# Optimization experiments

Measured on AMD Instinct MI355X. Metric: run time of the kernel, lower is better.

## Reference

```python
import jax, jax.numpy as jnp
import numpy as np

D_MODEL = 1024
N_HEADS = 16
HEAD_DIM = D_MODEL // N_HEADS


def setup_inputs() -> dict:
    key = jax.random.key(0)
    k0, k1, k2, k3, k4, k5 = jax.random.split(key, 6)
    s = 1.0 / np.sqrt(D_MODEL)
    return {
        "q": jax.random.normal(k0, (2, 2048, D_MODEL), dtype=jnp.float32),
        "Wq": jax.random.normal(k1, (D_MODEL, D_MODEL), dtype=jnp.float32) * s,
        "Wk": jax.random.normal(k2, (D_MODEL, D_MODEL), dtype=jnp.float32) * s,
        "Wv": jax.random.normal(k3, (D_MODEL, D_MODEL), dtype=jnp.float32) * s,
        "Wo": jax.random.normal(k4, (D_MODEL, D_MODEL), dtype=jnp.float32) * s,
        "bo": jax.random.normal(k5, (D_MODEL,), dtype=jnp.float32) * 0.01,
    }


def _split_heads(x):
    b, s, _ = x.shape
    return x.reshape(b, s, N_HEADS, HEAD_DIM).transpose(0, 2, 1, 3)  # [b,h,s,d]


def reference(q, Wq, Wk, Wv, Wo, bo):
    # self-attention: k = v = q
    qh = _split_heads(q @ Wq)  # [b,h,s,d]
    kh = _split_heads(q @ Wk)
    vh = _split_heads(q @ Wv)
    scale = 1.0 / np.sqrt(HEAD_DIM).astype(np.float32)
    scores = jnp.einsum("bhqd,bhkd->bhqk", qh, kh) * scale
    attn = jax.nn.softmax(scores, axis=-1)
    ctx = jnp.einsum("bhqk,bhkd->bhqd", attn, vh)
    b, h, s, d = ctx.shape
    ctx = ctx.transpose(0, 2, 1, 3).reshape(b, s, h * d)
    return ctx @ Wo + bo
```

## Files before the change

### kernel.cpp

```cpp
#include <hip/hip_runtime.h>
#include <cstdint>

typedef unsigned short u16;
typedef __bf16 bf16x8 __attribute__((ext_vector_type(8)));
typedef __bf16 bf16x2 __attribute__((ext_vector_type(2)));
typedef float floatx4 __attribute__((ext_vector_type(4)));
typedef unsigned short u16x4 __attribute__((ext_vector_type(4)));
typedef unsigned short u16x8 __attribute__((ext_vector_type(8)));

#define MFMA16(a, b, c) __builtin_amdgcn_mfma_f32_16x16x32_bf16((a), (b), (c), 0, 0, 0)
#define QSCALE_LOG2E 0.18033688011112042f


typedef __attribute__((address_space(3))) void as3_void;
typedef __attribute__((address_space(1))) void as1_void;

static __device__ __forceinline__ void async_load16(const void* g, void* l) {
  __builtin_amdgcn_global_load_lds((as1_void*)(uintptr_t)g, (as3_void*)(uintptr_t)l,
                                   16, 0, 0);
}

static __device__ __forceinline__ u16 f2bf(float f) {
  union { float f; unsigned int u; } v; v.f = f;
  unsigned int u = v.u;
  u += 0x7fffu + ((u >> 16) & 1u);
  return (u16)(u >> 16);
}

static __device__ __forceinline__ u16x4 pack_bf4(float a, float b, float c, float d) {
#if __has_builtin(__builtin_amdgcn_cvt_pk_bf16_f32)
  union { u16x4 v4; bf16x2 v2[2]; } u;
  u.v2[0] = __builtin_amdgcn_cvt_pk_bf16_f32(a, b);
  u.v2[1] = __builtin_amdgcn_cvt_pk_bf16_f32(c, d);
  return u.v4;
#else
  u16x4 r; r[0] = f2bf(a); r[1] = f2bf(b); r[2] = f2bf(c); r[3] = f2bf(d);
  return r;
#endif
}

static __device__ __forceinline__ float fast_exp2(float x) {
#if __has_builtin(__builtin_amdgcn_exp2f)
  return __builtin_amdgcn_exp2f(x);
#else
  return exp2f(x);
#endif
}


__global__ __launch_bounds__(256) void prep_kernel(
    const float* __restrict__ w0, const float* __restrict__ w1,
    const float* __restrict__ w2, const float* __restrict__ w3,
    u16* __restrict__ wout,
    const float* __restrict__ xin, u16* __restrict__ xout) {
  if (blockIdx.z == 4) {
    int blk = blockIdx.y * 16 + blockIdx.x;
    size_t base = (size_t)blk * 16384 + (size_t)threadIdx.x * 8;
#pragma unroll
    for (int r = 0; r < 8; r++) {
      size_t i = base + (size_t)r * 2048;
      float4 a = *(const float4*)(xin + i);
      float4 b = *(const float4*)(xin + i + 4);
      u16x8 o;
      o[0] = f2bf(a.x); o[1] = f2bf(a.y); o[2] = f2bf(a.z); o[3] = f2bf(a.w);
      o[4] = f2bf(b.x); o[5] = f2bf(b.y); o[6] = f2bf(b.z); o[7] = f2bf(b.w);
      *(u16x8*)(xout + i) = o;
    }
    return;
  }
  __shared__ u16 t[64][65];
  const float* in = (blockIdx.z == 0) ? w0 : (blockIdx.z == 1) ? w1
                    : (blockIdx.z == 2) ? w2 : w3;
  u16* oz = wout + (size_t)blockIdx.z * (1024 * 1024);
  const int tid = threadIdx.x;
  const int x = tid & 63, y0 = tid >> 6;
  const int bx = blockIdx.x * 64, by = blockIdx.y * 64;
#pragma unroll
  for (int p = 0; p < 16; p++) {
    int y = y0 + p * 4;
    t[y][x] = f2bf(in[(size_t)(by + y) * 1024 + bx + x]);
  }
  __syncthreads();
#pragma unroll
  for (int p = 0; p < 16; p++) {
    int r = y0 + p * 4;
    oz[(size_t)(bx + r) * 1024 + by + x] = t[x][r];
  }
}


__global__ __launch_bounds__(256) void vt_kernel(
    const u16* __restrict__ V, u16* __restrict__ VT) {
  __shared__ u16 t[64][65];
  const int bh = blockIdx.z, b = bh >> 4, h = bh & 15;
  const u16* iz = V + (size_t)b * 2048 * 1024 + h * 64;
  u16* oz = VT + (size_t)bh * 64 * 2048;
  const int tid = threadIdx.x;
  const int x = tid & 63, y0 = tid >> 6;
  const int by = blockIdx.y * 64;
#pragma unroll
  for (int p = 0; p < 16; p++) {
    int y = y0 + p * 4;
    t[y][x] = iz[(size_t)(by + y) * 1024 + x];
  }
  __syncthreads();
#pragma unroll
  for (int p = 0; p < 16; p++) {
    int r = y0 + p * 4;
    oz[(size_t)r * 2048 + by + x] = t[x][r];
  }
}


__global__ __launch_bounds__(256, 2) void gemm_bt_kernel(
    const u16* __restrict__ A, const u16* __restrict__ BT,
    const float* __restrict__ bias, void* __restrict__ out,
    int M, int N, int K, int mode) {
  __shared__ u16 As[128 * 32];
  __shared__ u16 Bs[128 * 32];
  const int tid = threadIdx.x;
  const int w = tid >> 6, lane = tid & 63;
  const int bm = blockIdx.y * 128, bn = blockIdx.x * 128;
  const int z = blockIdx.z;
  const u16* Bz = BT + (size_t)z * N * K;

  const int c0 = w * 2, c1 = c0 + 1;
  const int mA0 = c0 * 16 + (lane >> 2), mA1 = c1 * 16 + (lane >> 2);
  const int kg0 = (lane & 3) ^ ((mA0 >> 1) & 3);
  const int kg1 = (lane & 3) ^ ((mA1 >> 1) & 3);
  const u16* agp0 = A + (size_t)(bm + mA0) * K + kg0 * 8;
  const u16* agp1 = A + (size_t)(bm + mA1) * K + kg1 * 8;
  const u16* bgp0 = Bz + (size_t)(bn + mA0) * K + kg0 * 8;
  const u16* bgp1 = Bz + (size_t)(bn + mA1) * K + kg1 * 8;
  u16* ald0 = As + c0 * 512; u16* ald1 = As + c1 * 512;
  u16* bld0 = Bs + c0 * 512; u16* bld1 = Bs + c1 * 512;

  const int wm = (w >> 1) * 64, wn = (w & 1) * 64;
  floatx4 acc[4][4] = {};

  int a_off[4], b_off[4];
#pragma unroll
  for (int i = 0; i < 4; i++) {
    int m = wm + i * 16 + (lane & 15);
    a_off[i] = m * 32 + (((lane >> 4) ^ ((m >> 1) & 3)) * 8);
    int n = wn + i * 16 + (lane & 15);
    b_off[i] = n * 32 + (((lane >> 4) ^ ((n >> 1) & 3)) * 8);
  }

  for (int k0 = 0; k0 < K; k0 += 32) {
    __syncthreads();
    async_load16(agp0 + k0, ald0);
    async_load16(agp1 + k0, ald1);
    async_load16(bgp0 + k0, bld0);
    async_load16(bgp1 + k0, bld1);
    __syncthreads();
    bf16x8 af[4], bf[4];
#pragma unroll
    for (int i = 0; i < 4; i++) af[i] = *(const bf16x8*)(As + a_off[i]);
#pragma unroll
    for (int j = 0; j < 4; j++) bf[j] = *(const bf16x8*)(Bs + b_off[j]);
#pragma unroll
    for (int i = 0; i < 4; i++)
#pragma unroll
      for (int j = 0; j < 4; j++)
        acc[i][j] = MFMA16(af[i], bf[j], acc[i][j]);
  }

  const int roff = (lane >> 4) * 4;
  const int coff = lane & 15;
  if (mode == 0) {
    const float sc = (z == 0) ? QSCALE_LOG2E : 1.0f;
    u16* outz = (u16*)out + (size_t)z * M * N;
#pragma unroll
    for (int i = 0; i < 4; i++) {
      int r0 = bm + wm + i * 16 + roff;
#pragma unroll
      for (int j = 0; j < 4; j++) {
        int c = bn + wn + j * 16 + coff;
#pragma unroll
        for (int r = 0; r < 4; r++)
          outz[(size_t)(r0 + r) * N + c] = f2bf(acc[i][j][r] * sc);
      }
    }
  } else {
    float* outf = (float*)out;
#pragma unroll
    for (int i = 0; i < 4; i++) {
      int r0 = bm + wm + i * 16 + roff;
#pragma unroll
      for (int j = 0; j < 4; j++) {
        int c = bn + wn + j * 16 + coff;
        float bv = bias[c];
#pragma unroll
        for (int r = 0; r < 4; r++)
          outf[(size_t)(r0 + r) * N + c] = acc[i][j][r] + bv;
      }
    }
  }
}


__global__ __launch_bounds__(256, 2) void attn_kernel(
    const u16* __restrict__ Q, const u16* __restrict__ Kx,
    const u16* __restrict__ VT, u16* __restrict__ ctx) {
  __shared__ u16 Ks[128 * 64];
  __shared__ u16 Vs[64 * 128];
  __shared__ u16 Ps[4][32 * 136];
  const int tid = threadIdx.x;
  const int w = tid >> 6, lane = tid & 63;
  const int bh = blockIdx.y, b = bh >> 4, h = bh & 15;
  const int q0 = blockIdx.x * 128;
  const u16* Qh = Q + (size_t)b * 2048 * 1024 + h * 64;
  const u16* Kh = Kx + (size_t)b * 2048 * 1024 + h * 64;
  const u16* Vh = VT + (size_t)bh * 64 * 2048;

  const int qbase = q0 + w * 32;
  bf16x8 qf[2][2];
#pragma unroll
  for (int qt = 0; qt < 2; qt++)
#pragma unroll
    for (int ks = 0; ks < 2; ks++)
      qf[qt][ks] = *(const bf16x8*)(Qh + (size_t)(qbase + qt * 16 + (lane & 15)) * 1024 +
                                    ks * 32 + (lane >> 4) * 8);

  bf16x8 onesf;
#pragma unroll
  for (int i = 0; i < 8; i++) onesf[i] = (__bf16)1.0f;

  const u16* kgp[4]; const u16* vgp[4];
  u16* kld[4]; u16* vld[4];
#pragma unroll
  for (int i = 0; i < 4; i++) {
    int c = w * 4 + i;
    int sl = c * 8 + (lane >> 3);
    int dg = (lane & 7) ^ (lane >> 3);
    kgp[i] = Kh + (size_t)sl * 1024 + dg * 8;
    kld[i] = Ks + c * 512;
    int dl = c * 4 + (lane >> 4);
    int sg = (lane & 15) ^ (dl & 15);
    vgp[i] = Vh + (size_t)dl * 2048 + sg * 8;
    vld[i] = Vs + c * 512;
  }

  floatx4 o[2][4] = {};
  floatx4 lacc[2] = {};
  u16* Pw = Ps[w];

  for (int t = 0; t < 16; t++) {
    const int k0 = t * 128;
    __syncthreads();
#pragma unroll
    for (int i = 0; i < 4; i++) {
      async_load16(kgp[i] + (size_t)k0 * 1024, kld[i]);
      async_load16(vgp[i] + k0, vld[i]);
    }
    __syncthreads();

    floatx4 st[8][2];
#pragma unroll
    for (int si = 0; si < 8; si++) {
      st[si][0] = floatx4{0.f, 0.f, 0.f, 0.f};
      st[si][1] = floatx4{0.f, 0.f, 0.f, 0.f};
    }
#pragma unroll
    for (int ks = 0; ks < 2; ks++) {
#pragma unroll
      for (int si = 0; si < 8; si++) {
        int s = si * 16 + (lane & 15);
        int slot = ((ks * 4) + (lane >> 4)) ^ (s & 7);
        bf16x8 kf = *(const bf16x8*)(Ks + s * 64 + slot * 8);
        st[si][0] = MFMA16(kf, qf[0][ks], st[si][0]);
        st[si][1] = MFMA16(kf, qf[1][ks], st[si][1]);
      }
    }

#pragma unroll
    for (int qt = 0; qt < 2; qt++) {
      int q = qt * 16 + (lane & 15);
#pragma unroll
      for (int si = 0; si < 8; si++) {
        float p0 = fast_exp2(st[si][qt][0]);
        float p1 = fast_exp2(st[si][qt][1]);
        float p2 = fast_exp2(st[si][qt][2]);
        float p3 = fast_exp2(st[si][qt][3]);
        u16x4 pk = pack_bf4(p0, p1, p2, p3);
        *(u16x4*)(Pw + q * 136 + si * 16 + (lane >> 4) * 4) = pk;
      }
    }

#pragma unroll
    for (int ks = 0; ks < 4; ks++) {
      bf16x8 vf[4];
#pragma unroll
      for (int jt = 0; jt < 4; jt++) {
        int d = jt * 16 + (lane & 15);
        int slot = ((ks * 4) + (lane >> 4)) ^ (d & 15);
        vf[jt] = *(const bf16x8*)(Vs + d * 128 + slot * 8);
      }
#pragma unroll
      for (int qt = 0; qt < 2; qt++) {
        bf16x8 pf = *(const bf16x8*)(Pw + (qt * 16 + (lane & 15)) * 136 +
                                     ks * 32 + (lane >> 4) * 8);
#pragma unroll
        for (int jt = 0; jt < 4; jt++)
          o[qt][jt] = MFMA16(pf, vf[jt], o[qt][jt]);
        lacc[qt] = MFMA16(pf, onesf, lacc[qt]);
      }
    }
  }

#pragma unroll
  for (int qt = 0; qt < 2; qt++)
#pragma unroll
    for (int r = 0; r < 4; r++) {
      float inv = 1.0f / lacc[qt][r];
      int s = qbase + qt * 16 + (lane >> 4) * 4 + r;
#pragma unroll
      for (int j = 0; j < 4; j++) {
        int c = h * 64 + j * 16 + (lane & 15);
        ctx[(size_t)(b * 2048 + s) * 1024 + c] = f2bf(o[qt][j][r] * inv);
      }
    }
}


extern "C" void kernel_launch(void* const* d_in, const int* in_sizes, int n_in,
                              void* d_out, int out_size, void* d_ws, size_t ws_size,
                              hipStream_t stream) {
  (void)in_sizes; (void)n_in; (void)out_size; (void)ws_size;
  const float* x  = (const float*)d_in[0];
  const float* Wq = (const float*)d_in[1];
  const float* Wk = (const float*)d_in[2];
  const float* Wv = (const float*)d_in[3];
  const float* Wo = (const float*)d_in[4];
  const float* bo = (const float*)d_in[5];
  u16* ws = (u16*)d_ws;
  const size_t MM = 1024 * 1024;
  u16* WT  = ws;
  u16* WoT = ws + 3 * MM;
  u16* Xb  = ws + 4 * MM;
  u16* QKV = ws + 8 * MM;
  u16* VTp = ws + 20 * MM;
  u16* CTX = ws + 24 * MM;

  dim3 blk(256);
  prep_kernel<<<dim3(16, 16, 5), blk, 0, stream>>>(Wq, Wk, Wv, Wo, WT, x, Xb);
  gemm_bt_kernel<<<dim3(8, 32, 3), blk, 0, stream>>>(Xb, WT, nullptr, QKV,
                                                     4096, 1024, 1024, 0);
  vt_kernel<<<dim3(1, 32, 32), blk, 0, stream>>>(QKV + 8 * MM, VTp);
  attn_kernel<<<dim3(16, 32, 1), blk, 0, stream>>>(QKV, QKV + 4 * MM, VTp, CTX);
  gemm_bt_kernel<<<dim3(8, 32, 1), blk, 0, stream>>>(CTX, WoT, bo, d_out,
                                                     4096, 1024, 1024, 1);
}
```

Before: 197.7 us.

## Fuse V transpose into QKV GEMM epilogue, remap attention grid, restructure score loop

The QKV projection GEMM now writes the V output transposed per head straight into the VT buffer, which removes the separate vt_kernel launch and its round trip through memory. The attention grid is flattened to 1D and remapped so that groups of 8 heads share consecutive block ids, aiming for better K/V cache locality across concurrently running blocks. The QK^T score loop is restructured to compute, exponentiate and store P per 16-key tile with precomputed LDS base pointers, which shortens register live ranges. The GEMM launch bound is raised to 3 blocks per SM, which may force register spills.

```diff
diff --git a/kernel.cpp b/kernel.cpp
--- a/kernel.cpp
+++ b/kernel.cpp
@@ -89,32 +89,10 @@
 }
 
 
-__global__ __launch_bounds__(256) void vt_kernel(
-    const u16* __restrict__ V, u16* __restrict__ VT) {
-  __shared__ u16 t[64][65];
-  const int bh = blockIdx.z, b = bh >> 4, h = bh & 15;
-  const u16* iz = V + (size_t)b * 2048 * 1024 + h * 64;
-  u16* oz = VT + (size_t)bh * 64 * 2048;
-  const int tid = threadIdx.x;
-  const int x = tid & 63, y0 = tid >> 6;
-  const int by = blockIdx.y * 64;
-#pragma unroll
-  for (int p = 0; p < 16; p++) {
-    int y = y0 + p * 4;
-    t[y][x] = iz[(size_t)(by + y) * 1024 + x];
-  }
-  __syncthreads();
-#pragma unroll
-  for (int p = 0; p < 16; p++) {
-    int r = y0 + p * 4;
-    oz[(size_t)r * 2048 + by + x] = t[x][r];
-  }
-}
-
-
-__global__ __launch_bounds__(256, 2) void gemm_bt_kernel(
+__global__ __launch_bounds__(256, 3) void gemm_bt_kernel(
     const u16* __restrict__ A, const u16* __restrict__ BT,
     const float* __restrict__ bias, void* __restrict__ out,
+    u16* __restrict__ outVT,
     int M, int N, int K, int mode) {
   __shared__ u16 As[128 * 32];
   __shared__ u16 Bs[128 * 32];
@@ -169,17 +147,32 @@
   const int roff = (lane >> 4) * 4;
   const int coff = lane & 15;
   if (mode == 0) {
-    const float sc = (z == 0) ? QSCALE_LOG2E : 1.0f;
-    u16* outz = (u16*)out + (size_t)z * M * N;
-#pragma unroll
-    for (int i = 0; i < 4; i++) {
-      int r0 = bm + wm + i * 16 + roff;
-#pragma unroll
-      for (int j = 0; j < 4; j++) {
-        int c = bn + wn + j * 16 + coff;
-#pragma unroll
-        for (int r = 0; r < 4; r++)
-          outz[(size_t)(r0 + r) * N + c] = f2bf(acc[i][j][r] * sc);
+    if (z == 2) {
+#pragma unroll
+      for (int i = 0; i < 4; i++) {
+        int r0 = bm + wm + i * 16 + roff;
+        int b = r0 >> 11, s = r0 & 2047;
+#pragma unroll
+        for (int j = 0; j < 4; j++) {
+          int c = bn + wn + j * 16 + coff;
+          int h = c >> 6, d = c & 63;
+          u16x4 pk = pack_bf4(acc[i][j][0], acc[i][j][1], acc[i][j][2], acc[i][j][3]);
+          *(u16x4*)(outVT + ((size_t)(b * 16 + h) * 64 + d) * 2048 + s) = pk;
+        }
+      }
+    } else {
+      const float sc = (z == 0) ? QSCALE_LOG2E : 1.0f;
+      u16* outz = (u16*)out + (size_t)z * M * N;
+#pragma unroll
+      for (int i = 0; i < 4; i++) {
+        int r0 = bm + wm + i * 16 + roff;
+#pragma unroll
+        for (int j = 0; j < 4; j++) {
+          int c = bn + wn + j * 16 + coff;
+#pragma unroll
+          for (int r = 0; r < 4; r++)
+            outz[(size_t)(r0 + r) * N + c] = f2bf(acc[i][j][r] * sc);
+        }
       }
     }
   } else {
@@ -208,8 +201,10 @@
   __shared__ u16 Ps[4][32 * 136];
   const int tid = threadIdx.x;
   const int w = tid >> 6, lane = tid & 63;
-  const int bh = blockIdx.y, b = bh >> 4, h = bh & 15;
-  const int q0 = blockIdx.x * 128;
+  const int bid = blockIdx.x;
+  const int bh = (bid >> 7) * 8 + (bid & 7);
+  const int q0 = ((bid >> 3) & 15) * 128;
+  const int b = bh >> 4, h = bh & 15;
   const u16* Qh = Q + (size_t)b * 2048 * 1024 + h * 64;
   const u16* Kh = Kx + (size_t)b * 2048 * 1024 + h * 64;
   const u16* Vh = VT + (size_t)bh * 64 * 2048;
@@ -226,6 +221,7 @@
   bf16x8 onesf;
 #pragma unroll
   for (int i = 0; i < 8; i++) onesf[i] = (__bf16)1.0f;
+  const floatx4 zero4 = {};
 
   const u16* kgp[4]; const u16* vgp[4];
   u16* kld[4]; u16* vld[4];
@@ -242,6 +238,11 @@
     vld[i] = Vs + c * 512;
   }
 
+  const int slot_k0 = (lane >> 4) ^ (lane & 7);
+  const int slot_k1 = (4 + (lane >> 4)) ^ (lane & 7);
+  const u16* kf0_base = Ks + (lane & 15) * 64 + slot_k0 * 8;
+  const u16* kf1_base = Ks + (lane & 15) * 64 + slot_k1 * 8;
+
   floatx4 o[2][4] = {};
   floatx4 lacc[2] = {};
   u16* Pw = Ps[w];
@@ -256,36 +257,20 @@
     }
     __syncthreads();
 
-    floatx4 st[8][2];
 #pragma unroll
     for (int si = 0; si < 8; si++) {
-      st[si][0] = floatx4{0.f, 0.f, 0.f, 0.f};
-      st[si][1] = floatx4{0.f, 0.f, 0.f, 0.f};
-    }
-#pragma unroll
-    for (int ks = 0; ks < 2; ks++) {
-#pragma unroll
-      for (int si = 0; si < 8; si++) {
-        int s = si * 16 + (lane & 15);
-        int slot = ((ks * 4) + (lane >> 4)) ^ (s & 7);
-        bf16x8 kf = *(const bf16x8*)(Ks + s * 64 + slot * 8);
-        st[si][0] = MFMA16(kf, qf[0][ks], st[si][0]);
-        st[si][1] = MFMA16(kf, qf[1][ks], st[si][1]);
-      }
-    }
-
-#pragma unroll
-    for (int qt = 0; qt < 2; qt++) {
-      int q = qt * 16 + (lane & 15);
-#pragma unroll
-      for (int si = 0; si < 8; si++) {
-        float p0 = fast_exp2(st[si][qt][0]);
-        float p1 = fast_exp2(st[si][qt][1]);
-        float p2 = fast_exp2(st[si][qt][2]);
-        float p3 = fast_exp2(st[si][qt][3]);
-        u16x4 pk = pack_bf4(p0, p1, p2, p3);
-        *(u16x4*)(Pw + q * 136 + si * 16 + (lane >> 4) * 4) = pk;
-      }
+      bf16x8 kf0 = *(const bf16x8*)(kf0_base + si * 1024);
+      bf16x8 kf1 = *(const bf16x8*)(kf1_base + si * 1024);
+      floatx4 st0 = MFMA16(kf0, qf[0][0], zero4);
+      st0 = MFMA16(kf1, qf[0][1], st0);
+      floatx4 st1 = MFMA16(kf0, qf[1][0], zero4);
+      st1 = MFMA16(kf1, qf[1][1], st1);
+      u16x4 pk0 = pack_bf4(fast_exp2(st0[0]), fast_exp2(st0[1]),
+                           fast_exp2(st0[2]), fast_exp2(st0[3]));
+      u16x4 pk1 = pack_bf4(fast_exp2(st1[0]), fast_exp2(st1[1]),
+                           fast_exp2(st1[2]), fast_exp2(st1[3]));
+      *(u16x4*)(Pw + (lane & 15) * 136 + si * 16 + (lane >> 4) * 4) = pk0;
+      *(u16x4*)(Pw + (16 + (lane & 15)) * 136 + si * 16 + (lane >> 4) * 4) = pk1;
     }
 
 #pragma unroll
@@ -345,10 +330,9 @@
 
   dim3 blk(256);
   prep_kernel<<<dim3(16, 16, 5), blk, 0, stream>>>(Wq, Wk, Wv, Wo, WT, x, Xb);
-  gemm_bt_kernel<<<dim3(8, 32, 3), blk, 0, stream>>>(Xb, WT, nullptr, QKV,
+  gemm_bt_kernel<<<dim3(8, 32, 3), blk, 0, stream>>>(Xb, WT, nullptr, QKV, VTp,
                                                      4096, 1024, 1024, 0);
-  vt_kernel<<<dim3(1, 32, 32), blk, 0, stream>>>(QKV + 8 * MM, VTp);
-  attn_kernel<<<dim3(16, 32, 1), blk, 0, stream>>>(QKV, QKV + 4 * MM, VTp, CTX);
-  gemm_bt_kernel<<<dim3(8, 32, 1), blk, 0, stream>>>(CTX, WoT, bo, d_out,
+  attn_kernel<<<dim3(512, 1, 1), blk, 0, stream>>>(QKV, QKV + 4 * MM, VTp, CTX);
+  gemm_bt_kernel<<<dim3(8, 32, 1), blk, 0, stream>>>(CTX, WoT, bo, d_out, nullptr,
                                                      4096, 1024, 1024, 1);
 }
```

Result: no change. 194.5 us (-1.6%).
